# Optimization experiments

Hardware: AMD Instinct MI355X
Metric: run time of the kernel (lower is better)

Reference implementation:

```python
import jax, jax.numpy as jnp
import numpy as np


def setup_inputs() -> dict:
    key = jax.random.key(0)
    ks = jax.random.split(key, 8)
    batch, seqlen, nheads, headdim = 2, 2048, 64, 64
    ngroups, dstate = 1, 128
    x = jax.random.normal(ks[0], (batch, seqlen, nheads, headdim), jnp.float32)
    dt = jax.random.uniform(ks[1], (batch, seqlen, nheads), jnp.float32)
    # A must be negative for a stable decaying SSM
    A = -jax.random.uniform(ks[2], (nheads,), jnp.float32, minval=1.0, maxval=8.0)
    B = jax.random.normal(ks[3], (batch, seqlen, ngroups, dstate), jnp.float32)
    C = jax.random.normal(ks[4], (batch, seqlen, ngroups, dstate), jnp.float32)
    D = jax.random.uniform(ks[5], (nheads,), jnp.float32)
    z = jax.random.normal(ks[6], (batch, seqlen, nheads, headdim), jnp.float32)
    dt_bias = jax.random.uniform(ks[7], (nheads,), jnp.float32)
    return {"x": x, "dt": dt, "A": A, "B": B, "C": C, "D": D, "z": z,
            "dt_bias": dt_bias, "chunk_size": 256}


def _ssd_chunk_scan_combined(x, dt, A, B, C, D, z, dt_bias, chunk_size):
    batch, seqlen, nheads, headdim = x.shape
    ngroups, dstate = B.shape[2], B.shape[3]
    nchunks = seqlen // chunk_size  # seqlen chosen divisible by chunk_size

    # dt: (b, l, h) -> (b, h, c, s); bias + softplus, fp32
    dt = dt.astype(jnp.float32).reshape(batch, nchunks, chunk_size, nheads).transpose(0, 3, 1, 2)
    dt = jax.nn.softplus(dt + dt_bias.astype(jnp.float32)[None, :, None, None])
    dA = dt * A.astype(jnp.float32)[None, :, None, None]        # (b,h,c,s)
    dA_cumsum = jnp.cumsum(dA, axis=-1)                          # (b,h,c,s)

    # broadcast B/C groups to heads: 'b l g n -> b l (g h) n'
    rep = nheads // ngroups
    Bc = jnp.repeat(B, rep, axis=2).reshape(batch, nchunks, chunk_size, nheads, dstate)
    Cc = jnp.repeat(C, rep, axis=2).reshape(batch, nchunks, chunk_size, nheads, dstate)
    xc = x.reshape(batch, nchunks, chunk_size, nheads, headdim)

    # ---- chunk_state: per-chunk end-state contributions ----
    decay_states = jnp.exp(dA_cumsum[..., -1:] - dA_cumsum)      # (b,h,c,s)
    states = jnp.einsum('bcshn,bhcs,bcshp->bchpn', Bc, decay_states * dt, xc)

    # ---- state_passing: propagate states across chunks ----
    dA_last = dA_cumsum[..., -1]                                 # (b,h,c)
    csum = jnp.cumsum(jnp.pad(dA_last, ((0, 0), (0, 0), (1, 0))), axis=-1)  # (b,h,c+1)
    seg = csum[:, :, :, None] - csum[:, :, None, :]
    cmask = jnp.tril(jnp.ones((nchunks + 1, nchunks + 1), bool))
    decay_chunk = jnp.where(cmask, jnp.exp(seg), 0.0)            # (b,h,c+1,c+1)
    states_flat = states.reshape(batch, nchunks, nheads, headdim * dstate)
    states_cat = jnp.concatenate([jnp.zeros_like(states_flat[:, :1]), states_flat], axis=1)
    outs = jnp.einsum('bhzc,bchd->bzhd', decay_chunk, states_cat)
    prev_states = outs[:, :-1].reshape(batch, nchunks, nheads, headdim, dstate)
    final_states = outs[:, -1].reshape(batch, nheads, headdim, dstate)

    # ---- chunk_scan: intra-chunk attention-like scan + inter-chunk term ----
    CB = jnp.einsum('bclhn,bcshn->bchls', Cc, Bc)                # (b,c,h,l,s)
    decay = jnp.exp(dA_cumsum[:, :, :, :, None] - dA_cumsum[:, :, :, None, :])  # (b,h,c,l,s)
    scores = CB * decay.transpose(0, 2, 1, 3, 4)                 # (b,c,h,l,s)
    tri = jnp.tril(jnp.ones((chunk_size, chunk_size), bool))
    scores = jnp.where(tri, scores, 0.0)
    out = jnp.einsum('bchls,bhcs,bcshp->bclhp', scores, dt, xc)
    state_decay_out = jnp.exp(dA_cumsum).transpose(0, 2, 3, 1)[..., None]       # (b,c,l,h,1)
    out = out + jnp.einsum('bclhn,bchpn->bclhp', Cc, prev_states) * state_decay_out
    out = out.reshape(batch, seqlen, nheads, headdim)

    out = out + x * D[None, None, :, None]
    out = out * jax.nn.silu(z)
    return out.astype(x.dtype), final_states


def reference(x, dt, A, B, C, D, z, dt_bias, chunk_size):
    return _ssd_chunk_scan_combined(x, dt, A, B, C, D, z, dt_bias, chunk_size)
```

## Files before the change

kernel.cpp:

```cpp
#include <hip/hip_runtime.h>
#include <math.h>

#define BATCH 2
#define SEQ   2048
#define NH    64
#define HD    64
#define DS    128
#define CS    256
#define NC    8

typedef __attribute__((ext_vector_type(8))) short s16x8;
typedef __attribute__((ext_vector_type(4))) float f32x4;

#define MFMA16(a,b,c) __builtin_amdgcn_mfma_f32_16x16x32_bf16(a, b, c, 0, 0, 0)

__device__ inline unsigned short f2bf(float f) {
    unsigned u = __float_as_uint(f);
    return (unsigned short)((u + (0x7fffu + ((u >> 16) & 1u))) >> 16);
}
__device__ inline unsigned pack2bf(float a, float b) {
    return (unsigned)f2bf(a) | ((unsigned)f2bf(b) << 16);
}
__device__ inline float2 unpack2bf(unsigned u) {
    return make_float2(__uint_as_float(u << 16), __uint_as_float(u & 0xffff0000u));
}

__global__ __launch_bounds__(256) void k0a_xT(
    const float* __restrict__ x, unsigned* __restrict__ xT)
{
    int bid = blockIdx.x;
    int h = bid & 63, c = (bid >> 6) & 7, b = bid >> 9;
    int t = threadIdx.x;
    __shared__ float tile[64][65];
    for (int st = 0; st < 4; ++st) {
        int s0 = st * 64;
        __syncthreads();
        #pragma unroll
        for (int i = 0; i < 16; ++i) {
            int f = t + i * 256;
            int row = f >> 6, col = f & 63;
            tile[row][col] = x[((size_t)(b*SEQ + c*CS + s0 + row)*NH + h)*HD + col];
        }
        __syncthreads();
        #pragma unroll
        for (int i = 0; i < 8; ++i) {
            int f = t + i * 256;
            int p = f >> 5, sd = f & 31;
            xT[((size_t)bid*64 + p)*128 + (s0 >> 1) + sd] =
                pack2bf(tile[2*sd][p], tile[2*sd+1][p]);
        }
    }
}

__global__ __launch_bounds__(256) void k0b_cast(
    const float* __restrict__ src, unsigned* __restrict__ dst)
{
    size_t f = (size_t)blockIdx.x * 256 + threadIdx.x;
    const float4* s4 = (const float4*)(src + f * 8);
    float4 a = s4[0], bq = s4[1];
    uint4 o;
    o.x = pack2bf(a.x,  a.y);  o.y = pack2bf(a.z,  a.w);
    o.z = pack2bf(bq.x, bq.y); o.w = pack2bf(bq.z, bq.w);
    *(uint4*)(dst + f * 4) = o;
}

__global__ __launch_bounds__(256) void k0c_BT(
    const float* __restrict__ Bg, unsigned* __restrict__ BT)
{
    int bid = blockIdx.x;
    int st = bid & 3, nt = (bid >> 2) & 1, bc = bid >> 3;
    int b = bc >> 3, c = bc & 7;
    int s0 = st * 64, n0 = nt * 64;
    int t = threadIdx.x;
    __shared__ float tile[64][65];
    #pragma unroll
    for (int i = 0; i < 16; ++i) {
        int f = t + i * 256;
        int row = f >> 6, col = f & 63;
        tile[row][col] = Bg[(size_t)(b*SEQ + c*CS + s0 + row)*DS + n0 + col];
    }
    __syncthreads();
    #pragma unroll
    for (int i = 0; i < 8; ++i) {
        int f = t + i * 256;
        int n = f >> 5, sd = f & 31;
        BT[((size_t)bc*128 + n0 + n)*128 + (s0 >> 1) + sd] =
            pack2bf(tile[2*sd][n], tile[2*sd+1][n]);
    }
}

__global__ __launch_bounds__(CS) void k1_dt(
    const float* __restrict__ dt, const float* __restrict__ A,
    const float* __restrict__ dt_bias,
    float* __restrict__ dtp, float* __restrict__ dacs)
{
    int bid = blockIdx.x;
    int c = bid % NC;
    int h = (bid / NC) % NH;
    int b = bid / (NC * NH);
    int s = threadIdx.x;

    float v  = dt[((size_t)b * SEQ + c * CS + s) * NH + h] + dt_bias[h];
    float sp = fmaxf(v, 0.f) + log1pf(__expf(-fabsf(v)));
    float dA = sp * A[h];

    __shared__ float sm[CS];
    sm[s] = dA;
    __syncthreads();
    for (int off = 1; off < CS; off <<= 1) {
        float tt = (s >= off) ? sm[s - off] : 0.f;
        __syncthreads();
        sm[s] += tt;
        __syncthreads();
    }
    size_t o = (size_t)bid * CS + s;
    dtp[o]  = sp;
    dacs[o] = sm[s];
}

__global__ __launch_bounds__(256) void k2_cb(
    const float* __restrict__ Bg_, const float* __restrict__ Cg_,
    unsigned* __restrict__ cb_bf)
{
    const int TLt[10] = {0,1,1,2,2,2,3,3,3,3};
    const int TSt[10] = {0,0,1,0,1,2,0,1,2,3};
    int bid = blockIdx.x;
    int ti = bid % 10;
    int bc = bid / 10;
    int tl = TLt[ti], ts = TSt[ti];
    int b = bc / NC, c = bc % NC;

    const float* Cg = Cg_ + (size_t)(b * SEQ + c * CS + tl * 64) * DS;
    const float* Bg = Bg_ + (size_t)(b * SEQ + c * CS + ts * 64) * DS;

    __shared__ __align__(16) float Ct[32][68];
    __shared__ __align__(16) float Bt[32][68];

    int t  = threadIdx.x;
    int tx = t & 15, ty = t >> 4;
    int s0 = tx * 4, l0 = ty * 4;
    float acc[4][4] = {};

    for (int n0 = 0; n0 < DS; n0 += 32) {
        __syncthreads();
        {
            int r  = t >> 5;
            int nn = t & 31;
            #pragma unroll
            for (int i = 0; i < 8; ++i) {
                Ct[nn][r + i * 8] = Cg[(size_t)(r + i * 8) * DS + n0 + nn];
                Bt[nn][r + i * 8] = Bg[(size_t)(r + i * 8) * DS + n0 + nn];
            }
        }
        __syncthreads();
        #pragma unroll 8
        for (int n = 0; n < 32; ++n) {
            float4 cv = *(const float4*)&Ct[n][l0];
            float4 bv = *(const float4*)&Bt[n][s0];
            float cva[4] = {cv.x, cv.y, cv.z, cv.w};
            float bva[4] = {bv.x, bv.y, bv.z, bv.w};
            #pragma unroll
            for (int i = 0; i < 4; ++i)
                #pragma unroll
                for (int j = 0; j < 4; ++j)
                    acc[i][j] += cva[i] * bva[j];
        }
    }

    unsigned* cbg = cb_bf + (size_t)bc * 32768;
    #pragma unroll
    for (int i = 0; i < 4; ++i) {
        int row  = tl * 64 + l0 + i;
        int colb = (ts * 64 + s0) >> 1;
        uint2 wv;
        wv.x = pack2bf(acc[i][0], acc[i][1]);
        wv.y = pack2bf(acc[i][2], acc[i][3]);
        *(uint2*)&cbg[(size_t)row * 128 + colb] = wv;
    }
}

__global__ __launch_bounds__(256) void k3_chunk_state(
    const unsigned* __restrict__ xT, const unsigned* __restrict__ BT,
    const float* __restrict__ dtp, const float* __restrict__ dacs,
    float* __restrict__ states)
{
    int bid = blockIdx.x;
    int bc = bid >> 6;
    int h = bid & 63, c = (bid >> 6) & 7, b = bid >> 9;
    int t = threadIdx.x;
    int w = t >> 6, lane = t & 63, m16 = lane & 15, q = lane >> 4;

    size_t dt_base = ((size_t)(b*NH + h)*NC + c)*CS;
    float daL = dacs[dt_base + CS - 1];

    __shared__ unsigned xwS[64 * 36];
    __shared__ unsigned btS[128 * 36];
    __shared__ float coS[64];

    f32x4 acc[8] = {};

    for (int ks = 0; ks < 4; ++ks) {
        int s0 = ks * 64;
        __syncthreads();
        if (t < 64)
            coS[t] = dtp[dt_base + s0 + t] * __expf(daL - dacs[dt_base + s0 + t]);
        #pragma unroll
        for (int i = 0; i < 16; ++i) {
            int f = t + i * 256;
            int n = f >> 5, sd = f & 31;
            btS[n * 36 + sd] = BT[((size_t)bc*128 + n)*128 + (s0 >> 1) + sd];
        }
        __syncthreads();
        #pragma unroll
        for (int i = 0; i < 8; ++i) {
            int f = t + i * 256;
            int p = f >> 5, sd = f & 31;
            float2 v = unpack2bf(xT[((size_t)bid*64 + p)*128 + (s0 >> 1) + sd]);
            xwS[p * 36 + sd] = pack2bf(v.x * coS[2*sd], v.y * coS[2*sd + 1]);
        }
        __syncthreads();
        #pragma unroll
        for (int kk = 0; kk < 2; ++kk) {
            int kd = kk * 16 + q * 4;
            s16x8 af = *(const s16x8*)&xwS[(w*16 + m16)*36 + kd];
            #pragma unroll
            for (int nt = 0; nt < 8; ++nt) {
                s16x8 bfr = *(const s16x8*)&btS[(nt*16 + m16)*36 + kd];
                acc[nt] = MFMA16(af, bfr, acc[nt]);
            }
        }
    }

    float* sg = states + (size_t)bid * (HD * DS);
    #pragma unroll
    for (int nt = 0; nt < 8; ++nt) {
        #pragma unroll
        for (int r = 0; r < 4; ++r) {
            int p = w*16 + q*4 + r;
            sg[(size_t)p * 128 + nt*16 + m16] = acc[nt][r];
        }
    }
}

__global__ __launch_bounds__(256) void k4_state_passing(
    float* __restrict__ states, const float* __restrict__ dacs,
    float* __restrict__ final_states)
{
    int e = blockIdx.x * 256 + threadIdx.x;
    int n = e % DS;
    int p = (e / DS) % HD;
    int h = (e / (DS * HD)) % NH;
    int b = e / (DS * HD * NH);

    float r = 0.f;
    #pragma unroll
    for (int c = 0; c < NC; ++c) {
        size_t idx = (((size_t)(b * NC + c) * NH + h) * HD + p) * DS + n;
        float v = states[idx];
        states[idx] = r;
        float dal = dacs[((size_t)(b * NH + h) * NC + c) * CS + CS - 1];
        r = __expf(dal) * r + v;
    }
    final_states[((size_t)(b * NH + h) * HD + p) * DS + n] = r;
}

__global__ __launch_bounds__(256) void k5_chunk_scan(
    const float* __restrict__ x, const float* __restrict__ z,
    const unsigned* __restrict__ Cb, const float* __restrict__ Dp,
    const float* __restrict__ dtp, const float* __restrict__ dacs,
    const unsigned* __restrict__ cb_bf, const unsigned* __restrict__ xT,
    const float* __restrict__ prev, float* __restrict__ out)
{
    int bid = blockIdx.x;
    int h = bid & 63, c = (bid >> 6) & 7, b = bid >> 9;
    int bc = bid >> 6;
    int t = threadIdx.x;
    int w = t >> 6, lane = t & 63, m16 = lane & 15, q = lane >> 4;

    __shared__ unsigned Ws[256 * 36];
    __shared__ unsigned Xs[64 * 36];
    __shared__ float dacsS[CS], dtpS[CS], elS[CS];

    size_t dt_base = ((size_t)(b*NH + h)*NC + c)*CS;
    {
        float dv = dacs[dt_base + t];
        dacsS[t] = dv;
        elS[t]   = __expf(dv);
        dtpS[t]  = dtp[dt_base + t];
    }

    f32x4 acc[4][4] = {};

    for (int st = 0; st < 4; ++st) {
        int s0 = st * 64;
        int rows = 256 - s0;
        __syncthreads();
        for (int f = t; f < rows * 32; f += 256) {
            int r = f >> 5, sd = f & 31;
            int l = s0 + r;
            float2 v = unpack2bf(cb_bf[(size_t)bc*32768 + (size_t)l*128 + (s0 >> 1) + sd]);
            float dl = dacsS[l];
            int s = s0 + 2*sd;
            float w0 = (s     <= l) ? v.x * __expf(dl - dacsS[s])     * dtpS[s]     : 0.f;
            float w1 = (s + 1 <= l) ? v.y * __expf(dl - dacsS[s + 1]) * dtpS[s + 1] : 0.f;
            Ws[r * 36 + sd] = pack2bf(w0, w1);
        }
        #pragma unroll
        for (int i = 0; i < 8; ++i) {
            int f = t + i * 256;
            int p = f >> 5, sd = f & 31;
            Xs[p * 36 + sd] = xT[((size_t)bid*64 + p)*128 + (s0 >> 1) + sd];
        }
        __syncthreads();
        if (w >= st) {
            #pragma unroll
            for (int kk = 0; kk < 2; ++kk) {
                int kd = kk * 16 + q * 4;
                s16x8 bfr[4];
                #pragma unroll
                for (int pt = 0; pt < 4; ++pt)
                    bfr[pt] = *(const s16x8*)&Xs[(pt*16 + m16)*36 + kd];
                #pragma unroll
                for (int lt = 0; lt < 4; ++lt) {
                    s16x8 af = *(const s16x8*)&Ws[((w - st)*64 + lt*16 + m16)*36 + kd];
                    #pragma unroll
                    for (int pt = 0; pt < 4; ++pt)
                        acc[lt][pt] = MFMA16(af, bfr[pt], acc[lt][pt]);
                }
            }
        }
    }

    for (int kn = 0; kn < 2; ++kn) {
        __syncthreads();
        #pragma unroll
        for (int i = 0; i < 32; ++i) {
            int f = t + i * 256;
            int r = f >> 5, nd = f & 31;
            float2 v = unpack2bf(Cb[(size_t)(b*SEQ + c*CS + r)*64 + kn*32 + nd]);
            float el = elS[r];
            Ws[r * 36 + nd] = pack2bf(v.x * el, v.y * el);
        }
        #pragma unroll
        for (int i = 0; i < 8; ++i) {
            int f = t + i * 256;
            int p = f >> 5, nd = f & 31;
            float2 pv = *(const float2*)&prev[(size_t)bid*8192 + (size_t)p*128 + kn*64 + 2*nd];
            Xs[p * 36 + nd] = pack2bf(pv.x, pv.y);
        }
        __syncthreads();
        #pragma unroll
        for (int kk = 0; kk < 2; ++kk) {
            int kd = kk * 16 + q * 4;
            s16x8 bfr[4];
            #pragma unroll
            for (int pt = 0; pt < 4; ++pt)
                bfr[pt] = *(const s16x8*)&Xs[(pt*16 + m16)*36 + kd];
            #pragma unroll
            for (int lt = 0; lt < 4; ++lt) {
                s16x8 af = *(const s16x8*)&Ws[(w*64 + lt*16 + m16)*36 + kd];
                #pragma unroll
                for (int pt = 0; pt < 4; ++pt)
                    acc[lt][pt] = MFMA16(af, bfr[pt], acc[lt][pt]);
            }
        }
    }

    float Dh = Dp[h];
    #pragma unroll
    for (int lt = 0; lt < 4; ++lt) {
        #pragma unroll
        for (int r = 0; r < 4; ++r) {
            int l = w*64 + lt*16 + q*4 + r;
            size_t gro = ((size_t)(b*SEQ + c*CS + l)*NH + h)*HD;
            #pragma unroll
            for (int pt = 0; pt < 4; ++pt) {
                int p = pt*16 + m16;
                float xv = x[gro + p], zv = z[gro + p];
                float o = acc[lt][pt][r] + xv * Dh;
                float sig = 1.f / (1.f + __expf(-zv));
                out[gro + p] = o * (zv * sig);
            }
        }
    }
}

extern "C" void kernel_launch(void* const* d_in, const int* in_sizes, int n_in,
                              void* d_out, int out_size, void* d_ws, size_t ws_size,
                              hipStream_t stream)
{
    (void)in_sizes; (void)n_in; (void)out_size; (void)ws_size;
    const float* x       = (const float*)d_in[0];
    const float* dt      = (const float*)d_in[1];
    const float* A       = (const float*)d_in[2];
    const float* B       = (const float*)d_in[3];
    const float* C       = (const float*)d_in[4];
    const float* D       = (const float*)d_in[5];
    const float* z       = (const float*)d_in[6];
    const float* dt_bias = (const float*)d_in[7];

    float* out           = (float*)d_out;
    float* final_states  = out + (size_t)BATCH * SEQ * NH * HD;

    float* ws       = (float*)d_ws;
    float* dtp      = ws;
    float* dacs     = dtp + 262144;
    float* states   = dacs + 262144;
    unsigned* cb_bf = (unsigned*)(states + 8388608);
    unsigned* xT    = cb_bf + 524288;
    unsigned* BT    = xT + 8388608;
    unsigned* Cb    = BT + 262144;

    k0a_xT  <<<BATCH * NC * NH, 256, 0, stream>>>(x, xT);
    k0b_cast<<<256,             256, 0, stream>>>(C, Cb);
    k0c_BT  <<<BATCH * NC * 8,  256, 0, stream>>>(B, BT);
    k1_dt   <<<BATCH * NH * NC, CS,  0, stream>>>(dt, A, dt_bias, dtp, dacs);
    k2_cb   <<<BATCH * NC * 10, 256, 0, stream>>>(B, C, cb_bf);
    k3_chunk_state<<<BATCH * NC * NH, 256, 0, stream>>>(xT, BT, dtp, dacs, states);
    k4_state_passing<<<(BATCH * NH * HD * DS) / 256, 256, 0, stream>>>(states, dacs, final_states);
    k5_chunk_scan<<<BATCH * NC * NH, 256, 0, stream>>>(x, z, Cb, D, dtp, dacs,
                                                       cb_bf, xT, states, out);
}
```

Measured before the change: 398.3 us.

## Fold dt into x transpose, store states in bf16, load MFMA fragments directly

Runs the dt kernel first so the x transpose can pre-multiply x by softplus(dt), which removes the dtp loads from later kernels. Chunk states and the passed states are now stored as bf16 instead of fp32. The chunk_state and chunk_scan kernels drop their LDS staging and barriers and read MFMA fragments straight from global memory, applying the decay factors and causal mask in registers. chunk_scan also interleaves its row tiles across waves to balance the triangular work. The trade-off is extra bf16 rounding on the states and uncoalesced strided global loads in place of shared-memory reuse.

```diff
diff --git a/kernel.cpp b/kernel.cpp
--- a/kernel.cpp
+++ b/kernel.cpp
@@ -25,16 +25,51 @@
     return make_float2(__uint_as_float(u << 16), __uint_as_float(u & 0xffff0000u));
 }
 
-__global__ __launch_bounds__(256) void k0a_xT(
-    const float* __restrict__ x, unsigned* __restrict__ xT)
+union frag_u { unsigned u[4]; s16x8 v; };
+
+__global__ __launch_bounds__(CS) void k1_dt(
+    const float* __restrict__ dt, const float* __restrict__ A,
+    const float* __restrict__ dt_bias,
+    float* __restrict__ dtp, float* __restrict__ dacs)
+{
+    int bid = blockIdx.x;
+    int c = bid % NC;
+    int h = (bid / NC) % NH;
+    int b = bid / (NC * NH);
+    int s = threadIdx.x;
+
+    float v  = dt[((size_t)b * SEQ + c * CS + s) * NH + h] + dt_bias[h];
+    float sp = fmaxf(v, 0.f) + log1pf(__expf(-fabsf(v)));
+    float dA = sp * A[h];
+
+    __shared__ float sm[CS];
+    sm[s] = dA;
+    __syncthreads();
+    for (int off = 1; off < CS; off <<= 1) {
+        float tt = (s >= off) ? sm[s - off] : 0.f;
+        __syncthreads();
+        sm[s] += tt;
+        __syncthreads();
+    }
+    size_t o = (size_t)bid * CS + s;
+    dtp[o]  = sp;
+    dacs[o] = sm[s];
+}
+
+__global__ __launch_bounds__(256) void k0a_xdt(
+    const float* __restrict__ x, const float* __restrict__ dtp,
+    unsigned* __restrict__ xdt)
 {
     int bid = blockIdx.x;
     int h = bid & 63, c = (bid >> 6) & 7, b = bid >> 9;
     int t = threadIdx.x;
+    size_t dt_base = ((size_t)(b*NH + h)*NC + c)*CS;
     __shared__ float tile[64][65];
+    __shared__ float dtS[64];
     for (int st = 0; st < 4; ++st) {
         int s0 = st * 64;
         __syncthreads();
+        if (t < 64) dtS[t] = dtp[dt_base + s0 + t];
         #pragma unroll
         for (int i = 0; i < 16; ++i) {
             int f = t + i * 256;
@@ -46,8 +81,8 @@
         for (int i = 0; i < 8; ++i) {
             int f = t + i * 256;
             int p = f >> 5, sd = f & 31;
-            xT[((size_t)bid*64 + p)*128 + (s0 >> 1) + sd] =
-                pack2bf(tile[2*sd][p], tile[2*sd+1][p]);
+            xdt[((size_t)bid*64 + p)*128 + (s0 >> 1) + sd] =
+                pack2bf(tile[2*sd][p] * dtS[2*sd], tile[2*sd+1][p] * dtS[2*sd+1]);
         }
     }
 }
@@ -89,35 +124,6 @@
     }
 }
 
-__global__ __launch_bounds__(CS) void k1_dt(
-    const float* __restrict__ dt, const float* __restrict__ A,
-    const float* __restrict__ dt_bias,
-    float* __restrict__ dtp, float* __restrict__ dacs)
-{
-    int bid = blockIdx.x;
-    int c = bid % NC;
-    int h = (bid / NC) % NH;
-    int b = bid / (NC * NH);
-    int s = threadIdx.x;
-
-    float v  = dt[((size_t)b * SEQ + c * CS + s) * NH + h] + dt_bias[h];
-    float sp = fmaxf(v, 0.f) + log1pf(__expf(-fabsf(v)));
-    float dA = sp * A[h];
-
-    __shared__ float sm[CS];
-    sm[s] = dA;
-    __syncthreads();
-    for (int off = 1; off < CS; off <<= 1) {
-        float tt = (s >= off) ? sm[s - off] : 0.f;
-        __syncthreads();
-        sm[s] += tt;
-        __syncthreads();
-    }
-    size_t o = (size_t)bid * CS + s;
-    dtp[o]  = sp;
-    dacs[o] = sm[s];
-}
-
 __global__ __launch_bounds__(256) void k2_cb(
     const float* __restrict__ Bg_, const float* __restrict__ Cg_,
     unsigned* __restrict__ cb_bf)
@@ -180,9 +186,8 @@
 }
 
 __global__ __launch_bounds__(256) void k3_chunk_state(
-    const unsigned* __restrict__ xT, const unsigned* __restrict__ BT,
-    const float* __restrict__ dtp, const float* __restrict__ dacs,
-    float* __restrict__ states)
+    const unsigned* __restrict__ xdt, const unsigned* __restrict__ BT,
+    const float* __restrict__ dacs, unsigned short* __restrict__ states_bf)
 {
     int bid = blockIdx.x;
     int bc = bid >> 6;
@@ -191,85 +196,86 @@
     int w = t >> 6, lane = t & 63, m16 = lane & 15, q = lane >> 4;
 
     size_t dt_base = ((size_t)(b*NH + h)*NC + c)*CS;
-    float daL = dacs[dt_base + CS - 1];
-
-    __shared__ unsigned xwS[64 * 36];
-    __shared__ unsigned btS[128 * 36];
-    __shared__ float coS[64];
+    __shared__ float coS[CS];
+    {
+        float daL = dacs[dt_base + CS - 1];
+        coS[t] = __expf(daL - dacs[dt_base + t]);
+    }
+    __syncthreads();
+
+    const unsigned* xb = xdt + (size_t)bid * 8192;
+    const unsigned* bb = BT + (size_t)bc * 16384;
 
     f32x4 acc[8] = {};
 
+    #pragma unroll
     for (int ks = 0; ks < 4; ++ks) {
-        int s0 = ks * 64;
-        __syncthreads();
-        if (t < 64)
-            coS[t] = dtp[dt_base + s0 + t] * __expf(daL - dacs[dt_base + s0 + t]);
-        #pragma unroll
-        for (int i = 0; i < 16; ++i) {
-            int f = t + i * 256;
-            int n = f >> 5, sd = f & 31;
-            btS[n * 36 + sd] = BT[((size_t)bc*128 + n)*128 + (s0 >> 1) + sd];
-        }
-        __syncthreads();
-        #pragma unroll
-        for (int i = 0; i < 8; ++i) {
-            int f = t + i * 256;
-            int p = f >> 5, sd = f & 31;
-            float2 v = unpack2bf(xT[((size_t)bid*64 + p)*128 + (s0 >> 1) + sd]);
-            xwS[p * 36 + sd] = pack2bf(v.x * coS[2*sd], v.y * coS[2*sd + 1]);
-        }
-        __syncthreads();
         #pragma unroll
         for (int kk = 0; kk < 2; ++kk) {
-            int kd = kk * 16 + q * 4;
-            s16x8 af = *(const s16x8*)&xwS[(w*16 + m16)*36 + kd];
+            int kd = ks*32 + kk*16 + q*4;
+            int sbase = ks*64 + kk*32 + q*8;
+            uint4 xq = *(const uint4*)&xb[(w*16 + m16)*128 + kd];
+            float co8[8];
+            *(float4*)&co8[0] = *(const float4*)&coS[sbase];
+            *(float4*)&co8[4] = *(const float4*)&coS[sbase + 4];
+            frag_u af;
+            {
+                float2 v0 = unpack2bf(xq.x), v1 = unpack2bf(xq.y);
+                float2 v2 = unpack2bf(xq.z), v3 = unpack2bf(xq.w);
+                af.u[0] = pack2bf(v0.x*co8[0], v0.y*co8[1]);
+                af.u[1] = pack2bf(v1.x*co8[2], v1.y*co8[3]);
+                af.u[2] = pack2bf(v2.x*co8[4], v2.y*co8[5]);
+                af.u[3] = pack2bf(v3.x*co8[6], v3.y*co8[7]);
+            }
             #pragma unroll
             for (int nt = 0; nt < 8; ++nt) {
-                s16x8 bfr = *(const s16x8*)&btS[(nt*16 + m16)*36 + kd];
-                acc[nt] = MFMA16(af, bfr, acc[nt]);
-            }
-        }
-    }
-
-    float* sg = states + (size_t)bid * (HD * DS);
+                s16x8 bf8 = *(const s16x8*)&bb[(nt*16 + m16)*128 + kd];
+                acc[nt] = MFMA16(af.v, bf8, acc[nt]);
+            }
+        }
+    }
+
+    unsigned short* sg = states_bf + (size_t)bid * 8192;
     #pragma unroll
     for (int nt = 0; nt < 8; ++nt) {
         #pragma unroll
         for (int r = 0; r < 4; ++r) {
             int p = w*16 + q*4 + r;
-            sg[(size_t)p * 128 + nt*16 + m16] = acc[nt][r];
+            sg[p*128 + nt*16 + m16] = f2bf(acc[nt][r]);
         }
     }
 }
 
 __global__ __launch_bounds__(256) void k4_state_passing(
-    float* __restrict__ states, const float* __restrict__ dacs,
-    float* __restrict__ final_states)
+    const unsigned* __restrict__ states_bf, const float* __restrict__ dacs,
+    unsigned* __restrict__ prevT, float* __restrict__ final_states)
 {
     int e = blockIdx.x * 256 + threadIdx.x;
-    int n = e % DS;
-    int p = (e / DS) % HD;
-    int h = (e / (DS * HD)) % NH;
-    int b = e / (DS * HD * NH);
-
-    float r = 0.f;
+    int n2 = e & 63;
+    int p  = (e >> 6) & 63;
+    int h  = (e >> 12) & 63;
+    int b  = e >> 18;
+
+    float r0 = 0.f, r1 = 0.f;
     #pragma unroll
     for (int c = 0; c < NC; ++c) {
-        size_t idx = (((size_t)(b * NC + c) * NH + h) * HD + p) * DS + n;
-        float v = states[idx];
-        states[idx] = r;
-        float dal = dacs[((size_t)(b * NH + h) * NC + c) * CS + CS - 1];
-        r = __expf(dal) * r + v;
-    }
-    final_states[((size_t)(b * NH + h) * HD + p) * DS + n] = r;
+        size_t idx = (((size_t)(b*NC + c)*NH + h)*HD + p)*64 + n2;
+        float2 vv = unpack2bf(states_bf[idx]);
+        prevT[idx] = pack2bf(r0, r1);
+        float el = __expf(dacs[((size_t)(b*NH + h)*NC + c)*CS + CS - 1]);
+        r0 = el * r0 + vv.x;
+        r1 = el * r1 + vv.y;
+    }
+    float* fg = final_states + (((size_t)(b*NH + h)*HD + p)*DS + 2*n2);
+    fg[0] = r0; fg[1] = r1;
 }
 
 __global__ __launch_bounds__(256) void k5_chunk_scan(
     const float* __restrict__ x, const float* __restrict__ z,
     const unsigned* __restrict__ Cb, const float* __restrict__ Dp,
-    const float* __restrict__ dtp, const float* __restrict__ dacs,
-    const unsigned* __restrict__ cb_bf, const unsigned* __restrict__ xT,
-    const float* __restrict__ prev, float* __restrict__ out)
+    const float* __restrict__ dacs, const unsigned* __restrict__ cb_bf,
+    const unsigned* __restrict__ xdt, const unsigned* __restrict__ prevT,
+    float* __restrict__ out)
 {
     int bid = blockIdx.x;
     int h = bid & 63, c = (bid >> 6) & 7, b = bid >> 9;
@@ -277,107 +283,115 @@
     int t = threadIdx.x;
     int w = t >> 6, lane = t & 63, m16 = lane & 15, q = lane >> 4;
 
-    __shared__ unsigned Ws[256 * 36];
-    __shared__ unsigned Xs[64 * 36];
-    __shared__ float dacsS[CS], dtpS[CS], elS[CS];
-
+    __shared__ float dacsS[CS];
+    __shared__ float elS[CS];
     size_t dt_base = ((size_t)(b*NH + h)*NC + c)*CS;
     {
         float dv = dacs[dt_base + t];
         dacsS[t] = dv;
         elS[t]   = __expf(dv);
-        dtpS[t]  = dtp[dt_base + t];
-    }
+    }
+    __syncthreads();
+
+    const unsigned* xb  = xdt + (size_t)bid * 8192;
+    const unsigned* cbb = cb_bf + (size_t)bc * 32768;
 
     f32x4 acc[4][4] = {};
-
+    float dlv[4];
+    #pragma unroll
+    for (int jj = 0; jj < 4; ++jj) dlv[jj] = dacsS[(w + 4*jj)*16 + m16];
+
+    #pragma unroll
     for (int st = 0; st < 4; ++st) {
         int s0 = st * 64;
-        int rows = 256 - s0;
-        __syncthreads();
-        for (int f = t; f < rows * 32; f += 256) {
-            int r = f >> 5, sd = f & 31;
-            int l = s0 + r;
-            float2 v = unpack2bf(cb_bf[(size_t)bc*32768 + (size_t)l*128 + (s0 >> 1) + sd]);
-            float dl = dacsS[l];
-            int s = s0 + 2*sd;
-            float w0 = (s     <= l) ? v.x * __expf(dl - dacsS[s])     * dtpS[s]     : 0.f;
-            float w1 = (s + 1 <= l) ? v.y * __expf(dl - dacsS[s + 1]) * dtpS[s + 1] : 0.f;
-            Ws[r * 36 + sd] = pack2bf(w0, w1);
-        }
-        #pragma unroll
-        for (int i = 0; i < 8; ++i) {
-            int f = t + i * 256;
-            int p = f >> 5, sd = f & 31;
-            Xs[p * 36 + sd] = xT[((size_t)bid*64 + p)*128 + (s0 >> 1) + sd];
-        }
-        __syncthreads();
-        if (w >= st) {
-            #pragma unroll
-            for (int kk = 0; kk < 2; ++kk) {
-                int kd = kk * 16 + q * 4;
-                s16x8 bfr[4];
+        #pragma unroll
+        for (int kk = 0; kk < 2; ++kk) {
+            int kd = (s0 >> 1) + kk*16 + q*4;
+            s16x8 bfr[4];
+            #pragma unroll
+            for (int pt = 0; pt < 4; ++pt)
+                bfr[pt] = *(const s16x8*)&xb[(pt*16 + m16)*128 + kd];
+            int sbase = s0 + kk*32 + q*8;
+            float ds8[8];
+            *(float4*)&ds8[0] = *(const float4*)&dacsS[sbase];
+            *(float4*)&ds8[4] = *(const float4*)&dacsS[sbase + 4];
+            #pragma unroll
+            for (int jj = st; jj < 4; ++jj) {
+                if (st == jj && kk == 1 && w == 0) continue;
+                int lrow = (w + 4*jj)*16 + m16;
+                float dl = dlv[jj];
+                uint4 cbq = *(const uint4*)&cbb[(size_t)lrow*128 + kd];
+                frag_u af;
+                float2 v0 = unpack2bf(cbq.x), v1 = unpack2bf(cbq.y);
+                float2 v2 = unpack2bf(cbq.z), v3 = unpack2bf(cbq.w);
+                float wv[8];
+                wv[0] = v0.x * __expf(dl - ds8[0]);
+                wv[1] = v0.y * __expf(dl - ds8[1]);
+                wv[2] = v1.x * __expf(dl - ds8[2]);
+                wv[3] = v1.y * __expf(dl - ds8[3]);
+                wv[4] = v2.x * __expf(dl - ds8[4]);
+                wv[5] = v2.y * __expf(dl - ds8[5]);
+                wv[6] = v3.x * __expf(dl - ds8[6]);
+                wv[7] = v3.y * __expf(dl - ds8[7]);
+                if (st == jj) {
+                    #pragma unroll
+                    for (int j = 0; j < 8; ++j)
+                        wv[j] = (sbase + j <= lrow) ? wv[j] : 0.f;
+                }
+                af.u[0] = pack2bf(wv[0], wv[1]);
+                af.u[1] = pack2bf(wv[2], wv[3]);
+                af.u[2] = pack2bf(wv[4], wv[5]);
+                af.u[3] = pack2bf(wv[6], wv[7]);
                 #pragma unroll
                 for (int pt = 0; pt < 4; ++pt)
-                    bfr[pt] = *(const s16x8*)&Xs[(pt*16 + m16)*36 + kd];
-                #pragma unroll
-                for (int lt = 0; lt < 4; ++lt) {
-                    s16x8 af = *(const s16x8*)&Ws[((w - st)*64 + lt*16 + m16)*36 + kd];
-                    #pragma unroll
-                    for (int pt = 0; pt < 4; ++pt)
-                        acc[lt][pt] = MFMA16(af, bfr[pt], acc[lt][pt]);
-                }
-            }
-        }
-    }
-
-    for (int kn = 0; kn < 2; ++kn) {
-        __syncthreads();
-        #pragma unroll
-        for (int i = 0; i < 32; ++i) {
-            int f = t + i * 256;
-            int r = f >> 5, nd = f & 31;
-            float2 v = unpack2bf(Cb[(size_t)(b*SEQ + c*CS + r)*64 + kn*32 + nd]);
-            float el = elS[r];
-            Ws[r * 36 + nd] = pack2bf(v.x * el, v.y * el);
-        }
-        #pragma unroll
-        for (int i = 0; i < 8; ++i) {
-            int f = t + i * 256;
-            int p = f >> 5, nd = f & 31;
-            float2 pv = *(const float2*)&prev[(size_t)bid*8192 + (size_t)p*128 + kn*64 + 2*nd];
-            Xs[p * 36 + nd] = pack2bf(pv.x, pv.y);
-        }
-        __syncthreads();
-        #pragma unroll
-        for (int kk = 0; kk < 2; ++kk) {
-            int kd = kk * 16 + q * 4;
-            s16x8 bfr[4];
+                    acc[jj][pt] = MFMA16(af.v, bfr[pt], acc[jj][pt]);
+            }
+        }
+    }
+
+    {
+        const unsigned* pb = prevT + (size_t)bid * 4096;
+        float elv[4];
+        #pragma unroll
+        for (int jj = 0; jj < 4; ++jj) elv[jj] = elS[(w + 4*jj)*16 + m16];
+        #pragma unroll
+        for (int kq = 0; kq < 4; ++kq) {
+            int kd = kq*16 + q*4;
+            s16x8 pfr[4];
             #pragma unroll
             for (int pt = 0; pt < 4; ++pt)
-                bfr[pt] = *(const s16x8*)&Xs[(pt*16 + m16)*36 + kd];
-            #pragma unroll
-            for (int lt = 0; lt < 4; ++lt) {
-                s16x8 af = *(const s16x8*)&Ws[(w*64 + lt*16 + m16)*36 + kd];
+                pfr[pt] = *(const s16x8*)&pb[(pt*16 + m16)*64 + kd];
+            #pragma unroll
+            for (int jj = 0; jj < 4; ++jj) {
+                int lrow = (w + 4*jj)*16 + m16;
+                uint4 cq = *(const uint4*)&Cb[(size_t)(b*SEQ + c*CS + lrow)*64 + kd];
+                float el = elv[jj];
+                frag_u af;
+                float2 v0 = unpack2bf(cq.x), v1 = unpack2bf(cq.y);
+                float2 v2 = unpack2bf(cq.z), v3 = unpack2bf(cq.w);
+                af.u[0] = pack2bf(v0.x*el, v0.y*el);
+                af.u[1] = pack2bf(v1.x*el, v1.y*el);
+                af.u[2] = pack2bf(v2.x*el, v2.y*el);
+                af.u[3] = pack2bf(v3.x*el, v3.y*el);
                 #pragma unroll
                 for (int pt = 0; pt < 4; ++pt)
-                    acc[lt][pt] = MFMA16(af, bfr[pt], acc[lt][pt]);
+                    acc[jj][pt] = MFMA16(af.v, pfr[pt], acc[jj][pt]);
             }
         }
     }
 
     float Dh = Dp[h];
     #pragma unroll
-    for (int lt = 0; lt < 4; ++lt) {
+    for (int jj = 0; jj < 4; ++jj) {
         #pragma unroll
         for (int r = 0; r < 4; ++r) {
-            int l = w*64 + lt*16 + q*4 + r;
+            int l = (w + 4*jj)*16 + q*4 + r;
             size_t gro = ((size_t)(b*SEQ + c*CS + l)*NH + h)*HD;
             #pragma unroll
             for (int pt = 0; pt < 4; ++pt) {
                 int p = pt*16 + m16;
                 float xv = x[gro + p], zv = z[gro + p];
-                float o = acc[lt][pt][r] + xv * Dh;
+                float o = acc[jj][pt][r] + xv * Dh;
                 float sig = 1.f / (1.f + __expf(-zv));
                 out[gro + p] = o * (zv * sig);
             }
@@ -402,22 +416,24 @@
     float* out           = (float*)d_out;
     float* final_states  = out + (size_t)BATCH * SEQ * NH * HD;
 
-    float* ws       = (float*)d_ws;
-    float* dtp      = ws;
-    float* dacs     = dtp + 262144;
-    float* states   = dacs + 262144;
-    unsigned* cb_bf = (unsigned*)(states + 8388608);
-    unsigned* xT    = cb_bf + 524288;
-    unsigned* BT    = xT + 8388608;
-    unsigned* Cb    = BT + 262144;
-
-    k0a_xT  <<<BATCH * NC * NH, 256, 0, stream>>>(x, xT);
+    float* ws        = (float*)d_ws;
+    float* dtp       = ws;
+    float* dacs      = dtp + 262144;
+    unsigned short* states_bf = (unsigned short*)(dacs + 262144);
+    unsigned* prevT  = (unsigned*)(states_bf + 8388608);
+    unsigned* cb_bf  = prevT + 4194304;
+    unsigned* xdt    = cb_bf + 524288;
+    unsigned* BT     = xdt + 8388608;
+    unsigned* Cb     = BT + 262144;
+
+    k1_dt   <<<BATCH * NH * NC, CS,  0, stream>>>(dt, A, dt_bias, dtp, dacs);
+    k0a_xdt <<<BATCH * NC * NH, 256, 0, stream>>>(x, dtp, xdt);
     k0b_cast<<<256,             256, 0, stream>>>(C, Cb);
     k0c_BT  <<<BATCH * NC * 8,  256, 0, stream>>>(B, BT);
-    k1_dt   <<<BATCH * NH * NC, CS,  0, stream>>>(dt, A, dt_bias, dtp, dacs);
     k2_cb   <<<BATCH * NC * 10, 256, 0, stream>>>(B, C, cb_bf);
-    k3_chunk_state<<<BATCH * NC * NH, 256, 0, stream>>>(xT, BT, dtp, dacs, states);
-    k4_state_passing<<<(BATCH * NH * HD * DS) / 256, 256, 0, stream>>>(states, dacs, final_states);
-    k5_chunk_scan<<<BATCH * NC * NH, 256, 0, stream>>>(x, z, Cb, D, dtp, dacs,
-                                                       cb_bf, xT, states, out);
-}
+    k3_chunk_state<<<BATCH * NC * NH, 256, 0, stream>>>(xdt, BT, dacs, states_bf);
+    k4_state_passing<<<(BATCH * NH * HD * DS / 2) / 256, 256, 0, stream>>>(
+        (const unsigned*)states_bf, dacs, prevT, final_states);
+    k5_chunk_scan<<<BATCH * NC * NH, 256, 0, stream>>>(x, z, Cb, D, dacs,
+                                                       cb_bf, xdt, prevT, out);
+}
```

Result: faster. 336.1 us (-15.6%).
